# Kernel optimization log

Measured on AMD Instinct MI355X. Metric: run time of the kernel, lower is better.

Reference implementation:

```python
import jax, jax.numpy as jnp
import numpy as np

L, H, A, NREL2 = 3, 64, 64, 474
N_NODE, N_EDGE, B = 100000, 1000000, 32


def setup_inputs() -> dict:
    key = jax.random.key(0)
    ks = jax.random.split(key, 20)
    f = jax.random.normal
    s = 0.05
    return dict(
        sub_idx=jax.random.randint(ks[0], (N_EDGE,), 0, N_NODE),
        rel_idx=jax.random.randint(ks[1], (N_EDGE,), 0, NREL2),
        obj_idx=jax.random.randint(ks[2], (N_EDGE,), 0, N_NODE),
        edge_batch=jax.random.randint(ks[3], (N_EDGE,), 0, B),
        q_rel=jax.random.randint(ks[4], (B,), 0, NREL2),
        query_sub_idxs=jax.random.randint(ks[5], (B,), 0, N_NODE),
        rela_embed=f(ks[6], (L, NREL2, H)) * s,
        query_rela_embed=f(ks[7], (NREL2, H)) * s,
        Ws=f(ks[8], (L, H, A)) * s,
        Wr=f(ks[9], (L, H, A)) * s,
        Wqr=f(ks[10], (L, H, A)) * s,
        bqr=f(ks[11], (L, A)) * s,
        w_alpha=f(ks[12], (L, A)) * s,
        b_alpha=f(ks[13], (L,)) * s,
        W_h=f(ks[14], (L, H, H)) * s,
        gru_Wih=f(ks[15], (L, 3 * H, H)) * s,
        gru_Whh=f(ks[16], (L, 3 * H, H)) * s,
        gru_bih=f(ks[17], (L, 3 * H)) * s,
        gru_bhh=f(ks[18], (L, 3 * H)) * s,
        W_final=f(ks[19], (H,)) * s,
        n_node=N_NODE,
    )


def reference(sub_idx, rel_idx, obj_idx, edge_batch, q_rel, query_sub_idxs,
              rela_embed, query_rela_embed, Ws, Wr, Wqr, bqr, w_alpha, b_alpha,
              W_h, gru_Wih, gru_Whh, gru_bih, gru_bhh, W_final, n_node):
    # initializer='relation': seed query-subject nodes with query relation embedding
    hidden = jnp.zeros((n_node, H), jnp.float32).at[query_sub_idxs].set(query_rela_embed[q_rel])
    h0 = jnp.zeros((n_node, H), jnp.float32)  # GRU state

    for l in range(L):
        # ---- GNNLayer: gather -> attention MLP -> scatter-add ----
        hs = hidden[sub_idx]                       # [E, H]
        hr = rela_embed[l][rel_idx]                # [E, H]
        h_qr = rela_embed[l][q_rel][edge_batch]    # [E, H] query-rel emb per edge
        pre = jax.nn.relu(hs @ Ws[l] + hr @ Wr[l] + h_qr @ Wqr[l] + bqr[l])  # [E, A]
        alpha = jax.nn.sigmoid(pre @ w_alpha[l] + b_alpha[l])[:, None]       # [E, 1]
        msg = alpha * (hs * hr)                                              # [E, H]
        agg = jax.ops.segment_sum(msg, obj_idx, num_segments=n_node)        # [N, H]
        hidden = jax.nn.relu(agg @ W_h[l])

        # act_signal: mask untouched nodes (detached in original)
        mask = jnp.where(jax.lax.stop_gradient(jnp.sum(hidden, -1)) == 0, 0.0, 1.0)[:, None]

        # ---- one GRU step per node (PyTorch GRU math) ----
        gi = hidden @ gru_Wih[l].T + gru_bih[l]   # [N, 3H]
        gh = h0 @ gru_Whh[l].T + gru_bhh[l]       # [N, 3H]
        i_r, i_z, i_n = jnp.split(gi, 3, axis=-1)
        h_r, h_z, h_n = jnp.split(gh, 3, axis=-1)
        r = jax.nn.sigmoid(i_r + h_r)
        z = jax.nn.sigmoid(i_z + h_z)
        n = jnp.tanh(i_n + r * h_n)
        h_new = (1.0 - z) * n + z * h0
        hidden = h_new * mask
        h0 = h_new * mask

    # readout='linear', no bias
    scores = hidden @ W_final                     # [N]
    return scores
```

## Files before the change

kernel.cpp:

```cpp
#include <hip/hip_runtime.h>
#include <hip/hip_bf16.h>

#define NL 3
#define HD 64
#define TCAP 2048
#define NB 8

typedef unsigned char u8;

__device__ __forceinline__ float sigf(float x){ return 1.f/(1.f+__expf(-x)); }

__device__ __forceinline__ float wsum(float v){
  #pragma unroll
  for (int off=32; off; off>>=1) v += __shfl_xor(v, off, 64);
  return v;
}

__device__ __forceinline__ float bcastf(float v, int l){
  return __int_as_float(__builtin_amdgcn_readlane(__float_as_int(v), l));
}

__device__ __forceinline__ float ldin(const void* p, size_t i, int bf){
  return bf ? __bfloat162float(((const __hip_bfloat16*)p)[i]) : ((const float*)p)[i];
}

__device__ __forceinline__ int probe_bf(const void* probe, int lane){
  unsigned short h = ((const unsigned short*)probe)[lane];
  int e = (h >> 7) & 0xFF;
  int sane = ((h & 0x7FFF) == 0) || (e >= 96 && e <= 132);
  unsigned long long m = __ballot(sane != 0);
  return (__popcll(m) >= 56) ? 1 : 0;
}

__global__ void __launch_bounds__(256) k_setup(
    const void* __restrict__ W_h, const void* __restrict__ Ws,
    const void* __restrict__ Wih, const void* __restrict__ Whh,
    const void* __restrict__ bih, const void* __restrict__ bhh,
    const void* __restrict__ wal, const void* __restrict__ bal,
    const void* __restrict__ Wf,  const void* __restrict__ rel,
    const void* __restrict__ Wr,  const void* __restrict__ Wqr,
    const void* __restrict__ bqr, const void* __restrict__ qre,
    const int* __restrict__ q_rel, const int* __restrict__ qsub,
    float* __restrict__ WhF, float* __restrict__ WsF,
    float* __restrict__ WiT, float* __restrict__ WhT,
    float* __restrict__ biF, float* __restrict__ bhF,
    float* __restrict__ waF, float* __restrict__ baF,
    float* __restrict__ WfF, float* __restrict__ REL,
    float* __restrict__ R2, float* __restrict__ QR,
    float* __restrict__ hid, float* __restrict__ HS2, u8* __restrict__ liveB,
    int* __restrict__ stamp, int* __restrict__ plist, int* __restrict__ pcnt,
    int NR, int B, int PB, int TB)
{
  int lane = threadIdx.x & 63;
  int bf = probe_bf(rel, lane);

  if ((int)blockIdx.x < PB){
    int j = blockIdx.x*256 + threadIdx.x;
    const int sWT = NL*HD*HD, sWI = NL*192*HD, sB = NL*192;
    if (j < sWT){ WhF[j]=ldin(W_h,j,bf); return; } j-=sWT;
    if (j < sWT){ WsF[j]=ldin(Ws ,j,bf); return; } j-=sWT;
    if (j < sWI){ int l=j/(192*HD), q=j%(192*HD), h=q/192, a=q%192;
                  WiT[j]=ldin(Wih,(size_t)l*192*HD + (size_t)a*HD + h,bf); return; } j-=sWI;
    if (j < sWI){ int l=j/(192*HD), q=j%(192*HD), h=q/192, a=q%192;
                  WhT[j]=ldin(Whh,(size_t)l*192*HD + (size_t)a*HD + h,bf); return; } j-=sWI;
    if (j < sB){ biF[j]=ldin(bih,j,bf); return; } j-=sB;
    if (j < sB){ bhF[j]=ldin(bhh,j,bf); return; } j-=sB;
    if (j < NL*HD){ waF[j]=ldin(wal,j,bf); return; } j-=NL*HD;
    if (j < NL){ baF[j]=ldin(bal,j,bf); return; } j-=NL;
    if (j < HD){ WfF[j]=ldin(Wf,j,bf); return; } j-=HD;
    if (j < NL*NR*HD){ REL[j]=ldin(rel,j,bf); return; }
    return;
  }
  if ((int)blockIdx.x < PB+TB){
    int bid = ((int)blockIdx.x - PB)*4 + (threadIdx.x>>6);
    if (bid < NL*NR){
      int l = bid/NR, r = bid%NR;
      float x = ldin(rel,(size_t)(l*NR+r)*HD + lane,bf);
      float acc = 0.f;
      #pragma unroll
      for (int h=0; h<HD; ++h)
        acc = fmaf(bcastf(x, h), ldin(Wr,(size_t)(l*HD+h)*HD + lane,bf), acc);
      R2[(size_t)bid*HD + lane] = acc;
    } else if (bid < NL*NR + NL*B){
      int b2 = bid - NL*NR;
      int l = b2/B, b = b2%B;
      int r = q_rel[b];
      float x = ldin(rel,(size_t)(l*NR+r)*HD + lane,bf);
      float acc = ldin(bqr,(size_t)l*HD + lane,bf);
      #pragma unroll
      for (int h=0; h<HD; ++h)
        acc = fmaf(bcastf(x, h), ldin(Wqr,(size_t)(l*HD+h)*HD + lane,bf), acc);
      QR[(size_t)b2*HD + lane] = acc;
    }
    return;
  }
  int b = ((int)blockIdx.x - PB - TB)*4 + (threadIdx.x>>6);
  if (b >= B) return;
  int n = qsub[b];
  for (int b2 = b+1; b2 < B; ++b2) if (qsub[b2] == n) return;
  int r = q_rel[b];
  float v = ldin(qre,(size_t)r*HD + lane,bf);
  hid[(size_t)n*HD + lane] = v;
  float acc = 0.f;
  #pragma unroll 8
  for (int h=0; h<HD; ++h)
    acc = fmaf(bcastf(v,h), ldin(Ws,(size_t)h*HD + lane,bf), acc);
  HS2[(size_t)n*HD + lane] = acc;
  if (lane==0){
    liveB[n] = 1;
    stamp[n] = 1;
    int idx = atomicAdd(pcnt, 1);
    plist[idx] = n;
  }
}

__global__ void __launch_bounds__(256) k_edge(
    const int* __restrict__ sub, const int* __restrict__ rel_i,
    const int* __restrict__ obj, const int* __restrict__ eb,
    const u8* __restrict__ liveB,
    const float* __restrict__ hid, const float* __restrict__ HS2,
    const float* __restrict__ R2l, const float* __restrict__ QRl,
    const float* __restrict__ RELl, const float* __restrict__ waFl,
    const float* __restrict__ baFl, float* __restrict__ agg,
    int* __restrict__ stamp, int* __restrict__ tlist, int* __restrict__ tcnt,
    int ep, int E)
{
  __shared__ int s_cnt;
  __shared__ int s_base;
  __shared__ int s_buf[TCAP];
  if (threadIdx.x == 0) s_cnt = 0;
  __syncthreads();

  int lane = threadIdx.x & 63;
  int wid = (blockIdx.x*256 + threadIdx.x) >> 6;
  int nw = gridDim.x*4;
  float wa = waFl[lane];
  float ba = baFl[0];

  for (long long base = (long long)wid*256; base < E; base += (long long)nw*256){
    unsigned long long m[4];
    if (base + 256 <= E){
      int4 s4 = *reinterpret_cast<const int4*>(&sub[base + 4*(long long)lane]);
      m[0] = __ballot(liveB[s4.x] != 0);
      m[1] = __ballot(liveB[s4.y] != 0);
      m[2] = __ballot(liveB[s4.z] != 0);
      m[3] = __ballot(liveB[s4.w] != 0);
    } else {
      #pragma unroll
      for (int j=0;j<4;++j){
        long long e = base + 4*(long long)lane + j;
        bool lv = (e < E) && (liveB[sub[e]] != 0);
        m[j] = __ballot(lv);
      }
    }
    #pragma unroll
    for (int j=0;j<4;++j){
      unsigned long long mask = m[j];
      while (mask){
        int bit = (int)__ffsll(mask) - 1;
        mask &= mask - 1;
        long long ee = base + 4*(long long)bit + j;
        int ss = sub[ee], r = rel_i[ee], o = obj[ee], b = eb[ee];
        float hs  = hid[(size_t)ss*HD + lane];
        float pre = HS2[(size_t)ss*HD + lane] + R2l[(size_t)r*HD + lane] + QRl[(size_t)b*HD + lane];
        pre = fmaxf(pre, 0.f);
        float alpha = sigf(wsum(pre*wa) + ba);
        unsafeAtomicAdd(&agg[(size_t)o*HD + lane], alpha * hs * RELl[(size_t)r*HD + lane]);
        if (lane==0){
          int old = atomicExch(&stamp[o], ep);
          if (old != ep){
            int li = atomicAdd(&s_cnt, 1);
            if (li < TCAP) s_buf[li] = o;
            else { int gi = atomicAdd(tcnt, 1); tlist[gi] = o; }
          }
        }
      }
    }
  }

  __syncthreads();
  int cnt = s_cnt; if (cnt > TCAP) cnt = TCAP;
  if (threadIdx.x == 0 && cnt > 0) s_base = atomicAdd(tcnt, cnt);
  __syncthreads();
  if (cnt > 0){
    int b0 = s_base;
    for (int i = threadIdx.x; i < cnt; i += 256) tlist[b0 + i] = s_buf[i];
  }
}

__global__ void __launch_bounds__(256) k_node(
    const int* __restrict__ tlist, const int* __restrict__ tcnt,
    float* __restrict__ agg, float* __restrict__ hid, float* __restrict__ HS2,
    u8* __restrict__ liveB,
    const float* __restrict__ WhFl,
    const float* __restrict__ WiTl,
    const float* __restrict__ WhTl,
    const float* __restrict__ biFl, const float* __restrict__ bhFl,
    const float* __restrict__ WsFn,
    const float* __restrict__ WfF,
    const int* __restrict__ plist, const int* __restrict__ pcnt,
    const int* __restrict__ stamp,
    float* __restrict__ out, int N, int isFirst, int isLast, int ep)
{
  int cntv = tcnt[0]; if (cntv > N) cntv = N;
  int lane = threadIdx.x & 63;
  int wid = (blockIdx.x*256 + threadIdx.x) >> 6;
  int nw = gridDim.x*4;
  float bi0=biFl[lane], bi1=biFl[HD+lane], bi2=biFl[2*HD+lane];
  float bh0=bhFl[lane], bh1=bhFl[HD+lane], bh2=bhFl[2*HD+lane];
  float wfv = isLast ? WfF[lane] : 0.f;

  for (int i0 = wid*NB; i0 < cntv; i0 += nw*NB){
    int nd[NB]; bool val[NB]; bool wp[NB]; float av[NB];
    #pragma unroll
    for (int j=0;j<NB;++j){
      val[j] = (i0+j) < cntv;
      nd[j]  = tlist[val[j] ? (i0+j) : i0];
      wp[j]  = (!isFirst) && val[j] && (liveB[nd[j]] != 0);
      av[j]  = val[j] ? agg[(size_t)nd[j]*HD + lane] : 0.f;
    }
    if (!isLast){
      #pragma unroll
      for (int j=0;j<NB;++j) if (val[j]) agg[(size_t)nd[j]*HD + lane] = 0.f;
    }

    float hm[NB];
    #pragma unroll
    for (int j=0;j<NB;++j) hm[j] = 0.f;
    #pragma unroll 8
    for (int h=0; h<HD; ++h){
      float w = WhFl[h*HD + lane];
      #pragma unroll
      for (int j=0;j<NB;++j) hm[j] = fmaf(bcastf(av[j],h), w, hm[j]);
    }
    float mask[NB]; float h0v[NB];
    #pragma unroll
    for (int j=0;j<NB;++j){
      hm[j] = fmaxf(hm[j], 0.f);
      mask[j] = (__ballot(hm[j] != 0.f) != 0ull) ? 1.f : 0.f;
      h0v[j] = wp[j] ? hid[(size_t)nd[j]*HD + lane] : 0.f;
    }

    float gi0[NB], gi1[NB], gi2[NB], gh0[NB], gh1[NB], gh2[NB];
    #pragma unroll
    for (int j=0;j<NB;++j){ gi0[j]=bi0; gi1[j]=bi1; gi2[j]=bi2; gh0[j]=bh0; gh1[j]=bh1; gh2[j]=bh2; }
    #pragma unroll 4
    for (int h=0; h<HD; ++h){
      const float* __restrict__ wr = WiTl + (size_t)h*192;
      float w0 = wr[lane], w1 = wr[64+lane], w2 = wr[128+lane];
      #pragma unroll
      for (int j=0;j<NB;++j){
        float x = bcastf(hm[j],h);
        gi0[j] = fmaf(x, w0, gi0[j]);
        gi1[j] = fmaf(x, w1, gi1[j]);
        gi2[j] = fmaf(x, w2, gi2[j]);
      }
    }
    #pragma unroll
    for (int j=0;j<NB;++j){
      if (wp[j]){
        #pragma unroll 4
        for (int h=0; h<HD; ++h){
          const float* __restrict__ wr = WhTl + (size_t)h*192;
          float y = bcastf(h0v[j],h);
          gh0[j] = fmaf(y, wr[lane],     gh0[j]);
          gh1[j] = fmaf(y, wr[64+lane],  gh1[j]);
          gh2[j] = fmaf(y, wr[128+lane], gh2[j]);
        }
      }
    }

    float hn[NB];
    #pragma unroll
    for (int j=0;j<NB;++j){
      float r = sigf(gi0[j]+gh0[j]);
      float z = sigf(gi1[j]+gh1[j]);
      float nn = tanhf(gi2[j] + r*gh2[j]);
      hn[j] = ((1.f - z)*nn + z*h0v[j])*mask[j];
    }

    if (isLast){
      #pragma unroll
      for (int j=0;j<NB;++j){
        float sc = wsum(hn[j] * wfv);
        if (lane==0 && val[j]) out[nd[j]] = sc;
      }
      continue;
    }
    #pragma unroll
    for (int j=0;j<NB;++j){
      unsigned long long lv = __ballot(hn[j] != 0.f);
      if (val[j]){
        hid[(size_t)nd[j]*HD + lane] = hn[j];
        if (lane==0) liveB[nd[j]] = lv ? (u8)1 : (u8)0;
      }
    }

    float acc[NB];
    #pragma unroll
    for (int j=0;j<NB;++j) acc[j] = 0.f;
    #pragma unroll 8
    for (int h=0; h<HD; ++h){
      float w = WsFn[h*HD + lane];
      #pragma unroll
      for (int j=0;j<NB;++j) acc[j] = fmaf(bcastf(hn[j],h), w, acc[j]);
    }
    #pragma unroll
    for (int j=0;j<NB;++j) if (val[j]) HS2[(size_t)nd[j]*HD + lane] = acc[j];
  }

  if (!isLast){
    int pc = pcnt[0]; if (pc > N) pc = N;
    for (int i = blockIdx.x*256 + threadIdx.x; i < pc; i += gridDim.x*256){
      int n = plist[i];
      if (stamp[n] != ep) liveB[n] = 0;
    }
  }
}

extern "C" void kernel_launch(void* const* d_in, const int* in_sizes, int n_in,
                              void* d_out, int out_size, void* d_ws, size_t ws_size,
                              hipStream_t stream)
{
  const int* sub   = (const int*)d_in[0];
  const int* rel_i = (const int*)d_in[1];
  const int* obj   = (const int*)d_in[2];
  const int* eb    = (const int*)d_in[3];
  const int* q_rel = (const int*)d_in[4];
  const int* qsub  = (const int*)d_in[5];
  const void* rela = d_in[6];
  const void* qre  = d_in[7];
  const void* Wsp  = d_in[8];
  const void* Wr   = d_in[9];
  const void* Wqr  = d_in[10];
  const void* bqr  = d_in[11];
  const void* wal  = d_in[12];
  const void* bal  = d_in[13];
  const void* W_h  = d_in[14];
  const void* Wih  = d_in[15];
  const void* Whh  = d_in[16];
  const void* bih  = d_in[17];
  const void* bhh  = d_in[18];
  const void* Wf   = d_in[19];

  int E  = in_sizes[0];
  int B  = in_sizes[4];
  int NR = in_sizes[6]/(NL*HD);
  int N  = out_size;

  float* ws = (float*)d_ws;
  size_t o = 0;
  float* agg  = ws + o; o += (size_t)N*HD;
  int*   stamp= (int*)(ws + o); o += N;
  int*   cnts = (int*)(ws + o); o += 16;
  u8*    liveB= (u8*)(ws + o); o += (N+3)/4;
  float* hid  = ws + o; o += (size_t)N*HD;
  float* HS2  = ws + o; o += (size_t)N*HD;
  float* R2   = ws + o; o += (size_t)NL*NR*HD;
  float* QR   = ws + o; o += (size_t)NL*B*HD;
  float* REL  = ws + o; o += (size_t)NL*NR*HD;
  float* WhF  = ws + o; o += NL*HD*HD;
  float* WsF  = ws + o; o += NL*HD*HD;
  float* WiT  = ws + o; o += NL*192*HD;
  float* WhT  = ws + o; o += NL*192*HD;
  float* biF  = ws + o; o += NL*192;
  float* bhF  = ws + o; o += NL*192;
  float* waF  = ws + o; o += NL*HD;
  float* baF  = ws + o; o += NL;
  float* WfF  = ws + o; o += HD;
  int*   listA= (int*)(ws + o); o += N;
  int*   listB= (int*)(ws + o); o += N;

  size_t z1 = (size_t)N*HD*sizeof(float) + (size_t)N*sizeof(int)
            + 16*sizeof(int) + (size_t)((N+3)/4)*sizeof(float);
  hipMemsetAsync(agg, 0, z1, stream);
  hipMemsetAsync(d_out, 0, (size_t)N*sizeof(float), stream);

  int prepN = 2*(NL*HD*HD) + 2*(NL*192*HD) + 2*(NL*192) + NL*HD + NL + HD + NL*NR*HD;
  int PB = (prepN + 255)/256;
  int TB = (NL*NR + NL*B + 3)/4;
  int IB = (B + 3)/4;
  k_setup<<<PB + TB + IB, 256, 0, stream>>>(
      W_h, Wsp, Wih, Whh, bih, bhh, wal, bal, Wf, rela, Wr, Wqr, bqr, qre,
      q_rel, qsub,
      WhF, WsF, WiT, WhT, biF, bhF, waF, baF, WfF, REL, R2, QR,
      hid, HS2, liveB, stamp, listA, cnts+3, NR, B, PB, TB);

  int* curT = listB;
  int* prevL = listA;
  for (int l=0; l<NL; ++l){
    int ep = l + 2;
    k_edge<<<2048, 256, 0, stream>>>(sub, rel_i, obj, eb, liveB, hid, HS2,
        R2 + (size_t)l*NR*HD, QR + (size_t)l*B*HD, REL + (size_t)l*NR*HD,
        waF + l*HD, baF + l, agg, stamp, curT, cnts+4+l, ep, E);
    k_node<<<2048, 256, 0, stream>>>(curT, cnts+4+l, agg, hid, HS2, liveB,
        WhF + (size_t)l*HD*HD, WiT + (size_t)l*192*HD, WhT + (size_t)l*192*HD,
        biF + l*192, bhF + l*192,
        (l < NL-1) ? (WsF + (size_t)(l+1)*HD*HD) : WsF,
        WfF,
        prevL, (l==0) ? (cnts+3) : (cnts+4+l-1), stamp,
        (float*)d_out, N, (l==0)?1:0, (l==NL-1)?1:0, ep);
    int* t = prevL; prevL = curT; curT = t;
  }
}
```

Measured before the change: 175.5 us.

## Partition touched nodes by liveness and batch GRU hidden matmul across nodes

The edge kernel now splits newly touched target nodes into two lists: nodes that were already live go at the front of the list, newly activated nodes at the back. Counts are tracked separately, so the node kernel knows which nodes carry prior GRU state without reading liveB. The node kernel then runs the h0·Whh product once per group of nodes, sharing the weight loads across the group instead of repeating the loop per node. The edge scan also drops from 256 edges per wavefront with int4 index loads to 64 edges per wavefront, trading vectorized loads for finer-grained work, and it adds extra counter bookkeeping.

```diff
diff --git a/kernel.cpp b/kernel.cpp
--- a/kernel.cpp
+++ b/kernel.cpp
@@ -122,13 +122,14 @@
     const float* __restrict__ R2l, const float* __restrict__ QRl,
     const float* __restrict__ RELl, const float* __restrict__ waFl,
     const float* __restrict__ baFl, float* __restrict__ agg,
-    int* __restrict__ stamp, int* __restrict__ tlist, int* __restrict__ tcnt,
-    int ep, int E)
+    int* __restrict__ stamp, int* __restrict__ tlist,
+    int* __restrict__ tcA, int* __restrict__ tcB,
+    int ep, int E, int N)
 {
-  __shared__ int s_cnt;
-  __shared__ int s_base;
-  __shared__ int s_buf[TCAP];
-  if (threadIdx.x == 0) s_cnt = 0;
+  __shared__ int s_cntA, s_cntB, s_baseA, s_baseB;
+  __shared__ int s_bufA[TCAP];
+  __shared__ int s_bufB[TCAP];
+  if (threadIdx.x == 0){ s_cntA = 0; s_cntB = 0; }
   __syncthreads();
 
   int lane = threadIdx.x & 63;
@@ -137,41 +138,32 @@
   float wa = waFl[lane];
   float ba = baFl[0];
 
-  for (long long base = (long long)wid*256; base < E; base += (long long)nw*256){
-    unsigned long long m[4];
-    if (base + 256 <= E){
-      int4 s4 = *reinterpret_cast<const int4*>(&sub[base + 4*(long long)lane]);
-      m[0] = __ballot(liveB[s4.x] != 0);
-      m[1] = __ballot(liveB[s4.y] != 0);
-      m[2] = __ballot(liveB[s4.z] != 0);
-      m[3] = __ballot(liveB[s4.w] != 0);
-    } else {
-      #pragma unroll
-      for (int j=0;j<4;++j){
-        long long e = base + 4*(long long)lane + j;
-        bool lv = (e < E) && (liveB[sub[e]] != 0);
-        m[j] = __ballot(lv);
-      }
-    }
-    #pragma unroll
-    for (int j=0;j<4;++j){
-      unsigned long long mask = m[j];
-      while (mask){
-        int bit = (int)__ffsll(mask) - 1;
-        mask &= mask - 1;
-        long long ee = base + 4*(long long)bit + j;
-        int ss = sub[ee], r = rel_i[ee], o = obj[ee], b = eb[ee];
-        float hs  = hid[(size_t)ss*HD + lane];
-        float pre = HS2[(size_t)ss*HD + lane] + R2l[(size_t)r*HD + lane] + QRl[(size_t)b*HD + lane];
-        pre = fmaxf(pre, 0.f);
-        float alpha = sigf(wsum(pre*wa) + ba);
-        unsafeAtomicAdd(&agg[(size_t)o*HD + lane], alpha * hs * RELl[(size_t)r*HD + lane]);
-        if (lane==0){
-          int old = atomicExch(&stamp[o], ep);
-          if (old != ep){
-            int li = atomicAdd(&s_cnt, 1);
-            if (li < TCAP) s_buf[li] = o;
-            else { int gi = atomicAdd(tcnt, 1); tlist[gi] = o; }
+  for (long long base = (long long)wid*64; base < E; base += (long long)nw*64){
+    long long e = base + lane;
+    int s = (e < E) ? sub[e] : 0;
+    bool liv = (e < E) && (liveB[s] != 0);
+    unsigned long long mask = __ballot(liv);
+    while (mask){
+      int bit = (int)__ffsll(mask) - 1;
+      mask &= mask - 1;
+      long long ee = base + bit;
+      int ss = sub[ee], r = rel_i[ee], o = obj[ee], b = eb[ee];
+      float hs  = hid[(size_t)ss*HD + lane];
+      float pre = HS2[(size_t)ss*HD + lane] + R2l[(size_t)r*HD + lane] + QRl[(size_t)b*HD + lane];
+      pre = fmaxf(pre, 0.f);
+      float alpha = sigf(wsum(pre*wa) + ba);
+      unsafeAtomicAdd(&agg[(size_t)o*HD + lane], alpha * hs * RELl[(size_t)r*HD + lane]);
+      if (lane==0){
+        int old = atomicExch(&stamp[o], ep);
+        if (old != ep){
+          if (liveB[o]){
+            int li = atomicAdd(&s_cntA, 1);
+            if (li < TCAP) s_bufA[li] = o;
+            else { int gi = atomicAdd(tcA, 1); tlist[gi] = o; }
+          } else {
+            int li = atomicAdd(&s_cntB, 1);
+            if (li < TCAP) s_bufB[li] = o;
+            else { int gi = atomicAdd(tcB, 1); tlist[N-1-gi] = o; }
           }
         }
       }
@@ -179,17 +171,20 @@
   }
 
   __syncthreads();
-  int cnt = s_cnt; if (cnt > TCAP) cnt = TCAP;
-  if (threadIdx.x == 0 && cnt > 0) s_base = atomicAdd(tcnt, cnt);
+  int cA = s_cntA; if (cA > TCAP) cA = TCAP;
+  int cB = s_cntB; if (cB > TCAP) cB = TCAP;
+  if (threadIdx.x == 0){
+    if (cA) s_baseA = atomicAdd(tcA, cA);
+    if (cB) s_baseB = atomicAdd(tcB, cB);
+  }
   __syncthreads();
-  if (cnt > 0){
-    int b0 = s_base;
-    for (int i = threadIdx.x; i < cnt; i += 256) tlist[b0 + i] = s_buf[i];
-  }
+  int bA = s_baseA, bB = s_baseB;
+  for (int i = threadIdx.x; i < cA; i += 256) tlist[bA + i] = s_bufA[i];
+  for (int i = threadIdx.x; i < cB; i += 256) tlist[N-1-(bB + i)] = s_bufB[i];
 }
 
 __global__ void __launch_bounds__(256) k_node(
-    const int* __restrict__ tlist, const int* __restrict__ tcnt,
+    const int* __restrict__ tlist, const int* __restrict__ tcA, const int* __restrict__ tcB,
     float* __restrict__ agg, float* __restrict__ hid, float* __restrict__ HS2,
     u8* __restrict__ liveB,
     const float* __restrict__ WhFl,
@@ -198,11 +193,13 @@
     const float* __restrict__ biFl, const float* __restrict__ bhFl,
     const float* __restrict__ WsFn,
     const float* __restrict__ WfF,
-    const int* __restrict__ plist, const int* __restrict__ pcnt,
+    const int* __restrict__ prevL, const int* __restrict__ pcA, const int* __restrict__ pcB,
     const int* __restrict__ stamp,
     float* __restrict__ out, int N, int isFirst, int isLast, int ep)
 {
-  int cntv = tcnt[0]; if (cntv > N) cntv = N;
+  int cA = tcA[0]; if (cA > N) cA = N;
+  int cB = tcB[0]; if (cB > N) cB = N;
+  int cntv = cA + cB; if (cntv > N) cntv = N;
   int lane = threadIdx.x & 63;
   int wid = (blockIdx.x*256 + threadIdx.x) >> 6;
   int nw = gridDim.x*4;
@@ -214,9 +211,11 @@
     int nd[NB]; bool val[NB]; bool wp[NB]; float av[NB];
     #pragma unroll
     for (int j=0;j<NB;++j){
-      val[j] = (i0+j) < cntv;
-      nd[j]  = tlist[val[j] ? (i0+j) : i0];
-      wp[j]  = (!isFirst) && val[j] && (liveB[nd[j]] != 0);
+      int idx = i0+j;
+      val[j] = idx < cntv;
+      int ii = val[j] ? idx : 0;
+      nd[j]  = (ii < cA) ? tlist[ii] : tlist[N-1-(ii-cA)];
+      wp[j]  = (!isFirst) && val[j] && (ii < cA);
       av[j]  = val[j] ? agg[(size_t)nd[j]*HD + lane] : 0.f;
     }
     if (!isLast){
@@ -234,11 +233,13 @@
       for (int j=0;j<NB;++j) hm[j] = fmaf(bcastf(av[j],h), w, hm[j]);
     }
     float mask[NB]; float h0v[NB];
+    bool anyWp = false;
     #pragma unroll
     for (int j=0;j<NB;++j){
       hm[j] = fmaxf(hm[j], 0.f);
       mask[j] = (__ballot(hm[j] != 0.f) != 0ull) ? 1.f : 0.f;
       h0v[j] = wp[j] ? hid[(size_t)nd[j]*HD + lane] : 0.f;
+      anyWp |= wp[j];
     }
 
     float gi0[NB], gi1[NB], gi2[NB], gh0[NB], gh1[NB], gh2[NB];
@@ -256,16 +257,19 @@
         gi2[j] = fmaf(x, w2, gi2[j]);
       }
     }
-    #pragma unroll
-    for (int j=0;j<NB;++j){
-      if (wp[j]){
-        #pragma unroll 4
-        for (int h=0; h<HD; ++h){
-          const float* __restrict__ wr = WhTl + (size_t)h*192;
-          float y = bcastf(h0v[j],h);
-          gh0[j] = fmaf(y, wr[lane],     gh0[j]);
-          gh1[j] = fmaf(y, wr[64+lane],  gh1[j]);
-          gh2[j] = fmaf(y, wr[128+lane], gh2[j]);
+    if (anyWp){
+      #pragma unroll 4
+      for (int h=0; h<HD; ++h){
+        const float* __restrict__ wr = WhTl + (size_t)h*192;
+        float w0 = wr[lane], w1 = wr[64+lane], w2 = wr[128+lane];
+        #pragma unroll
+        for (int j=0;j<NB;++j){
+          if (wp[j]){
+            float y = bcastf(h0v[j],h);
+            gh0[j] = fmaf(y, w0, gh0[j]);
+            gh1[j] = fmaf(y, w1, gh1[j]);
+            gh2[j] = fmaf(y, w2, gh2[j]);
+          }
         }
       }
     }
@@ -310,9 +314,11 @@
   }
 
   if (!isLast){
-    int pc = pcnt[0]; if (pc > N) pc = N;
+    int pA = pcA[0]; if (pA > N) pA = N;
+    int pB = pcB[0]; if (pB > N) pB = N;
+    int pc = pA + pB; if (pc > N) pc = N;
     for (int i = blockIdx.x*256 + threadIdx.x; i < pc; i += gridDim.x*256){
-      int n = plist[i];
+      int n = (i < pA) ? prevL[i] : prevL[N-1-(i-pA)];
       if (stamp[n] != ep) liveB[n] = 0;
     }
   }
@@ -392,13 +398,16 @@
     int ep = l + 2;
     k_edge<<<2048, 256, 0, stream>>>(sub, rel_i, obj, eb, liveB, hid, HS2,
         R2 + (size_t)l*NR*HD, QR + (size_t)l*B*HD, REL + (size_t)l*NR*HD,
-        waF + l*HD, baF + l, agg, stamp, curT, cnts+4+l, ep, E);
-    k_node<<<2048, 256, 0, stream>>>(curT, cnts+4+l, agg, hid, HS2, liveB,
+        waF + l*HD, baF + l, agg, stamp, curT, cnts+l, cnts+4+l, ep, E, N);
+    k_node<<<2048, 256, 0, stream>>>(curT, cnts+l, cnts+4+l, agg, hid, HS2, liveB,
         WhF + (size_t)l*HD*HD, WiT + (size_t)l*192*HD, WhT + (size_t)l*192*HD,
         biF + l*192, bhF + l*192,
         (l < NL-1) ? (WsF + (size_t)(l+1)*HD*HD) : WsF,
         WfF,
-        prevL, (l==0) ? (cnts+3) : (cnts+4+l-1), stamp,
+        prevL,
+        (l==0) ? (cnts+3) : (cnts+(l-1)),
+        (l==0) ? (cnts+7) : (cnts+4+(l-1)),
+        stamp,
         (float*)d_out, N, (l==0)?1:0, (l==NL-1)?1:0, ep);
     int* t = prevL; prevL = curT; curT = t;
   }
```

New measurement: 232.0 us. 1.32x slower.
